# Kernel optimization log

Measured on AMD Instinct MI355X. Metric: run time of the kernel, lower is better.

## Reference

```python
import jax, jax.numpy as jnp
import numpy as np

EPS = 1e-5
SIGMA = 1.0

def _conv(x, w, stride):
    return jax.lax.conv_general_dilated(
        x, w, window_strides=(stride, stride),
        padding=[(w.shape[2] // 2, w.shape[2] // 2), (w.shape[3] // 2, w.shape[3] // 2)],
        dimension_numbers=('NCHW', 'OIHW', 'NCHW'))

def _bn(x, gamma, beta, mean, var):
    # inference-mode batchnorm over channel dim (NCHW)
    inv = gamma / jnp.sqrt(var + EPS)
    return x * inv[None, :, None, None] + (beta - mean * inv)[None, :, None, None]

def setup_inputs() -> dict:
    key = jax.random.key(0)
    ks = jax.random.split(key, 8)
    B, M, H, W, K = 8, 128, 64, 64, 6
    x = jax.random.normal(ks[0], (B, M, H, W), jnp.float32)
    cf = jax.random.normal(ks[1], (B, M, H, W), jnp.float32)
    w1 = jax.random.normal(ks[2], (M // 2, M, 3, 3), jnp.float32) * 0.05
    w2 = jax.random.normal(ks[3], (M // 4, M // 2, 3, 3), jnp.float32) * 0.05
    w3 = jax.random.normal(ks[4], (K, M // 4, 1, 1), jnp.float32) * 0.05
    def bn_params(k, c):
        k1, k2 = jax.random.split(k)
        return (jnp.ones((c,), jnp.float32),
                jnp.zeros((c,), jnp.float32),
                jax.random.normal(k1, (c,), jnp.float32) * 0.1,
                jnp.abs(jax.random.normal(k2, (c,), jnp.float32)) * 0.1 + 1.0)
    g1, b1, m1, v1 = bn_params(ks[5], M // 2)
    g2, b2, m2, v2 = bn_params(ks[6], M // 4)
    g3, b3, m3, v3 = bn_params(ks[7], K)
    return dict(x=x, center_features=cf, w1=w1, g1=g1, b1=b1, m1=m1, v1=v1,
                w2=w2, g2=g2, b2=b2, m2=m2, v2=v2,
                w3=w3, g3=g3, b3=b3, m3=m3, v3=v3)

def reference(x, center_features, w1, g1, b1, m1, v1, w2, g2, b2, m2, v2, w3, g3, b3, m3, v3):
    # center branch: conv-bn-relu x2 (stride 2) + 1x1 conv-bn, then spatial mean
    c = jax.nn.relu(_bn(_conv(center_features, w1, 2), g1, b1, m1, v1))
    c = jax.nn.relu(_bn(_conv(c, w2, 2), g2, b2, m2, v2))
    c = _bn(_conv(c, w3, 1), g3, b3, m3, v3)
    centers = c.reshape(c.shape[0], c.shape[1], -1).mean(axis=2)  # [B, K]

    B, C, H, W = x.shape
    K = centers.shape[-1]
    xf = x.reshape(B, C, H * W, 1)                      # [B,C,HW,1]
    cb = centers[:, None, None, :]                      # [B,1,1,K]
    dist = (xf - cb) ** 2                               # [B,C,HW,K]
    phi_soft = jax.nn.softmax(-SIGMA * dist, axis=-1)
    qsoft = jnp.sum(phi_soft * cb, axis=-1).reshape(B, C, H, W)
    symbols = jnp.argmin(dist, axis=-1)                 # [B,C,HW] (== argmax of hard softmax)
    qhard = centers[jnp.arange(B)[:, None, None], symbols].reshape(B, C, H, W)
    qbar = qsoft + jax.lax.stop_gradient(qhard - qsoft)
    return qbar, qsoft, qhard, symbols.reshape(B, C, H, W), centers
```

## Files before the change

### kernel.cpp

```cpp
#include <hip/hip_runtime.h>
#include <math.h>

#define BN_EPS 1e-5
#define SIGMA 1.0f

typedef double f64x4 __attribute__((ext_vector_type(4)));

__global__ __launch_bounds__(256, 4) void conv1_mfma_kernel(
    const float* __restrict__ in, const float* __restrict__ w1,
    float* __restrict__ part)
{
    __shared__ float swt[9216];

    int bid = blockIdx.x;
    int mt  = bid & 15;
    int b   = (bid >> 4) & 7;
    int ksp = bid >> 7;

    int tid = threadIdx.x;
    int l   = tid & 63;
    int wv  = tid >> 6;
    int wm  = wv >> 1;
    int wn  = wv & 1;
    int lc  = l & 15;
    int lg  = l >> 4;

    double ap = (double)lc;
    double bp = (l == 0) ? 1.0 : 0.0;
    f64x4 dp = {0., 0., 0., 0.};
    dp = __builtin_amdgcn_mfma_f64_16x16x4f64(ap, bp, dp, 0, 0, 0);
    int row0[4];
    #pragma unroll
    for (int r = 0; r < 4; ++r)
        row0[r] = ((int)__shfl(dp[r], (l & 0x30), 64)) & 15;

    for (int i = tid; i < 9216; i += 256) {
        int g   = i & 3;
        int n   = (i >> 2) & 63;
        int kic = i >> 8;
        int khw = kic >> 2;
        int icb = kic & 3;
        swt[i] = w1[(n * 128 + ksp * 16 + icb * 4 + g) * 9 + khw];
    }
    __syncthreads();

    f64x4 d00 = {0., 0., 0., 0.}, d01 = {0., 0., 0., 0.};
    f64x4 d10 = {0., 0., 0., 0.}, d11 = {0., 0., 0., 0.};

    const float* cb = in + (size_t)(b * 128 + ksp * 16 + lg) * 4096;
    int r0 = 4 * mt + 2 * wm - 1;
    const float* pbase = cb + (ptrdiff_t)(r0 * 64 + 2 * lc - 1);
    bool c0ok = (lc != 0);

    const float* pB = swt + (wn * 32 + lc) * 4 + lg;

    #pragma unroll
    for (int khw = 0; khw < 9; ++khw) {
        const int kh = khw / 3;
        const int kw = khw - 3 * kh;
        bool rowok = (kh > 0) || (r0 >= 0);
        #pragma unroll
        for (int icb = 0; icb < 4; ++icb) {
            const int offA = icb * 16384 + kh * 64 + kw;
            bool ok0 = rowok && ((kw > 0) || c0ok);
            const float* q0 = ok0 ? (pbase + offA) : cb;
            float f0 = *q0;
            double a0 = ok0 ? (double)f0 : 0.0;
            const float* q1 = rowok ? (pbase + offA + 32) : cb;
            float f1 = *q1;
            double a1 = rowok ? (double)f1 : 0.0;

            const int offB = (khw * 4 + icb) * 256;
            double b0 = (double)pB[offB];
            double b1 = (double)pB[offB + 64];

            d00 = __builtin_amdgcn_mfma_f64_16x16x4f64(a0, b0, d00, 0, 0, 0);
            d01 = __builtin_amdgcn_mfma_f64_16x16x4f64(a0, b1, d01, 0, 0, 0);
            d10 = __builtin_amdgcn_mfma_f64_16x16x4f64(a1, b0, d10, 0, 0, 0);
            d11 = __builtin_amdgcn_mfma_f64_16x16x4f64(a1, b1, d11, 0, 0, 0);
        }
    }

    __syncthreads();
    float* so = swt;
    #pragma unroll
    for (int mi = 0; mi < 2; ++mi) {
        f64x4 v0 = mi ? d10 : d00;
        f64x4 v1 = mi ? d11 : d01;
        #pragma unroll
        for (int r = 0; r < 4; ++r) {
            int m   = wm * 32 + mi * 16 + row0[r];
            int oc0 = wn * 32 + lc;
            so[oc0 * 65 + m]        = (float)v0[r];
            so[(oc0 + 16) * 65 + m] = (float)v1[r];
        }
    }
    __syncthreads();
    int oh0 = 2 * mt;
    for (int i = tid; i < 4096; i += 256) {
        int oc = i >> 6;
        int m  = i & 63;
        part[(size_t)ksp * 524288 +
             ((b * 64 + oc) * 32 + oh0 + (m >> 5)) * 32 + (m & 31)] = so[oc * 65 + m];
    }
}

__global__ __launch_bounds__(256) void conv2_partial_kernel(
    const float* __restrict__ part1,
    const float* __restrict__ g1, const float* __restrict__ be1,
    const float* __restrict__ mn1, const float* __restrict__ vr1,
    const float* __restrict__ w,
    float* __restrict__ part)
{
    __shared__ float tin[4][33][36];
    __shared__ float twt[4][9][8];
    __shared__ double sinv[4], ssh[4];

    int bid = blockIdx.x;
    int ocg = bid & 3;
    int b   = (bid >> 2) & 7;
    int isp = bid >> 5;

    int tid = threadIdx.x;
    int ow  = tid & 15;
    int oh  = tid >> 4;

    if (tid < 4) {
        int ch = isp * 4 + tid;
        double inv = (double)g1[ch] / sqrt((double)vr1[ch] + BN_EPS);
        sinv[tid] = inv;
        ssh[tid]  = (double)be1[ch] - (double)mn1[ch] * inv;
    }
    __syncthreads();

    for (int lin = tid; lin < 4 * 33 * 34; lin += 256) {
        int c   = lin % 34;
        int t2  = lin / 34;
        int rr  = t2 % 33;
        int icc = t2 / 33;
        int ih  = rr - 1;
        int iw  = c - 1;
        float v = 0.f;
        if ((unsigned)ih < 32u && (unsigned)iw < 32u) {
            int ch  = isp * 4 + icc;
            int idx = ((b * 64 + ch) * 32 + ih) * 32 + iw;
            double s = 0.0;
            #pragma unroll
            for (int p = 0; p < 8; ++p) s += (double)part1[idx + p * 524288];
            double o = s * sinv[icc] + ssh[icc];
            v = fmaxf((float)o, 0.f);
        }
        tin[icc][rr][c] = v;
    }
    for (int i = tid; i < 288; i += 256) {
        int j   = i & 7;
        int k   = (i >> 3) % 9;
        int icc = i / 72;
        twt[icc][k][j] = w[(ocg * 8 + j) * 576 + (isp * 4 + icc) * 9 + k];
    }
    __syncthreads();

    double acc[8];
    #pragma unroll
    for (int j = 0; j < 8; ++j) acc[j] = 0.0;

    for (int icc = 0; icc < 4; ++icc) {
        double xv[9];
        #pragma unroll
        for (int kh = 0; kh < 3; ++kh)
            #pragma unroll
            for (int kw = 0; kw < 3; ++kw)
                xv[kh * 3 + kw] = (double)tin[icc][2 * oh + kh][2 * ow + kw];
        #pragma unroll
        for (int k = 0; k < 9; ++k) {
            float4 wa = *(const float4*)&twt[icc][k][0];
            float4 wb = *(const float4*)&twt[icc][k][4];
            acc[0] = fma(xv[k], (double)wa.x, acc[0]);
            acc[1] = fma(xv[k], (double)wa.y, acc[1]);
            acc[2] = fma(xv[k], (double)wa.z, acc[2]);
            acc[3] = fma(xv[k], (double)wa.w, acc[3]);
            acc[4] = fma(xv[k], (double)wb.x, acc[4]);
            acc[5] = fma(xv[k], (double)wb.y, acc[5]);
            acc[6] = fma(xv[k], (double)wb.z, acc[6]);
            acc[7] = fma(xv[k], (double)wb.w, acc[7]);
        }
    }
    int obase = ((b * 32 + ocg * 8) * 16 + oh) * 16 + ow;
    #pragma unroll
    for (int j = 0; j < 8; ++j)
        part[isp * 65536 + obase + j * 256] = (float)acc[j];
}

__global__ __launch_bounds__(256) void conv2_combine_ybar_kernel(
    const float* __restrict__ part,
    const float* __restrict__ g, const float* __restrict__ be,
    const float* __restrict__ mn, const float* __restrict__ vr,
    double* __restrict__ ybar)
{
    __shared__ double sm[4];
    int j  = blockIdx.x;
    int oc = j & 31;
    int t  = threadIdx.x;
    int idx = j * 256 + t;
    double s = 0.0;
    #pragma unroll
    for (int p = 0; p < 16; ++p) s += (double)part[idx + p * 65536];
    double inv = (double)g[oc] / sqrt((double)vr[oc] + BN_EPS);
    double o = s * inv + ((double)be[oc] - (double)mn[oc] * inv);
    double v = fmax(o, 0.0);
    #pragma unroll
    for (int off = 32; off > 0; off >>= 1) v += __shfl_down(v, off, 64);
    if ((t & 63) == 0) sm[t >> 6] = v;
    __syncthreads();
    if (t == 0) ybar[j] = (sm[0] + sm[1] + sm[2] + sm[3]) * (1.0 / 256.0);
}

__global__ __launch_bounds__(64) void centers_kernel(
    const double* __restrict__ ybar, const float* __restrict__ w3,
    const float* __restrict__ g, const float* __restrict__ be,
    const float* __restrict__ mn, const float* __restrict__ vr,
    double* __restrict__ cen_ws, float* __restrict__ cen_out)
{
    int t = threadIdx.x;
    if (t < 48) {
        int b = t / 6;
        int k = t % 6;
        double acc = 0.0;
        for (int ic = 0; ic < 32; ++ic) acc = fma((double)w3[k * 32 + ic], ybar[b * 32 + ic], acc);
        double inv = (double)g[k] / sqrt((double)vr[k] + BN_EPS);
        double c = acc * inv + ((double)be[k] - (double)mn[k] * inv);
        cen_ws[t]  = c;
        cen_out[t] = (float)c;
    }
}

__global__ __launch_bounds__(256) void quant_kernel(
    const float* __restrict__ x, const double* __restrict__ centers,
    float* __restrict__ qbar, float* __restrict__ qsoft,
    float* __restrict__ qhard, float* __restrict__ sym)
{
    int vid = blockIdx.x * 256 + threadIdx.x;
    int b = vid >> 17;

    double c[6];
    float cf[6];
    #pragma unroll
    for (int k = 0; k < 6; ++k) { c[k] = centers[b * 6 + k]; cf[k] = (float)c[k]; }

    float4 xv = ((const float4*)x)[vid];
    float xs[4] = {xv.x, xv.y, xv.z, xv.w};
    float r_bar[4], r_soft[4], r_hard[4], r_sym[4];

    #pragma unroll
    for (int i = 0; i < 4; ++i) {
        double xx = (double)xs[i];
        double d[6];
        double dmin = 1e300;
        int amin = 0;
        #pragma unroll
        for (int k = 0; k < 6; ++k) {
            double t = xx - c[k];
            d[k] = t * t;
            if (d[k] < dmin) { dmin = d[k]; amin = k; }
        }
        float se = 0.f, sw = 0.f;
        #pragma unroll
        for (int k = 0; k < 6; ++k) {
            float e = __expf(SIGMA * (float)(dmin - d[k]));
            se += e;
            sw += e * cf[k];
        }
        float qs = sw / se;
        float qh = cf[amin];
        r_soft[i] = qs;
        r_hard[i] = qh;
        r_bar[i]  = qh;
        r_sym[i]  = (float)amin;
    }

    ((float4*)qbar)[vid]  = make_float4(r_bar[0],  r_bar[1],  r_bar[2],  r_bar[3]);
    ((float4*)qsoft)[vid] = make_float4(r_soft[0], r_soft[1], r_soft[2], r_soft[3]);
    ((float4*)qhard)[vid] = make_float4(r_hard[0], r_hard[1], r_hard[2], r_hard[3]);
    ((float4*)sym)[vid]   = make_float4(r_sym[0],  r_sym[1],  r_sym[2],  r_sym[3]);
}

extern "C" void kernel_launch(void* const* d_in, const int* in_sizes, int n_in,
                              void* d_out, int out_size, void* d_ws, size_t ws_size,
                              hipStream_t stream) {
    const float* x  = (const float*)d_in[0];
    const float* cf = (const float*)d_in[1];
    const float* w1 = (const float*)d_in[2];
    const float* g1 = (const float*)d_in[3];
    const float* b1 = (const float*)d_in[4];
    const float* m1 = (const float*)d_in[5];
    const float* v1 = (const float*)d_in[6];
    const float* w2 = (const float*)d_in[7];
    const float* g2 = (const float*)d_in[8];
    const float* b2 = (const float*)d_in[9];
    const float* m2 = (const float*)d_in[10];
    const float* v2 = (const float*)d_in[11];
    const float* w3 = (const float*)d_in[12];
    const float* g3 = (const float*)d_in[13];
    const float* b3 = (const float*)d_in[14];
    const float* m3 = (const float*)d_in[15];
    const float* v3 = (const float*)d_in[16];

    const int NELEM = 8 * 128 * 64 * 64;
    float* out   = (float*)d_out;
    float* qbar  = out;
    float* qsoft = out + (size_t)NELEM;
    float* qhard = out + (size_t)2 * NELEM;
    float* sym   = out + (size_t)3 * NELEM;
    float* cen_o = out + (size_t)4 * NELEM;

    char* ws = (char*)d_ws;
    float*  part1 = (float*)(ws);
    float*  part2 = (float*)(ws + 16777216);
    double* yb    = (double*)(ws + 20971520);
    double* cen   = (double*)(ws + 20973568);

    conv1_mfma_kernel<<<1024, 256, 0, stream>>>(cf, w1, part1);
    conv2_partial_kernel<<<512, 256, 0, stream>>>(part1, g1, b1, m1, v1, w2, part2);
    conv2_combine_ybar_kernel<<<256, 256, 0, stream>>>(part2, g2, b2, m2, v2, yb);
    centers_kernel<<<1, 64, 0, stream>>>(yb, w3, g3, b3, m3, v3, cen, cen_o);
    quant_kernel<<<NELEM / 4 / 256, 256, 0, stream>>>(x, cen, qbar, qsoft, qhard, sym);
}
```

Before: 187.9 us.

## Split conv1 work between FP64 MFMA blocks and scalar FP64 FMA blocks

Conv1 now launches a hybrid grid. Half the blocks keep the FP64 MFMA path for input-channel splits 4-7. The other half compute splits 0-3 with scalar double FMAs: weights are staged in LDS as doubles and input rows are register-prefetched. The aim is to use both the MFMA units and the vector ALUs at once, since the FP64 matrix path alone caps throughput. The cost is a scalar path with heavy register use and uneven per-block work, which could unbalance the blocks or lower occupancy.

```diff
diff --git a/kernel.cpp b/kernel.cpp
--- a/kernel.cpp
+++ b/kernel.cpp
@@ -6,102 +6,191 @@
 
 typedef double f64x4 __attribute__((ext_vector_type(4)));
 
-__global__ __launch_bounds__(256, 4) void conv1_mfma_kernel(
+__global__ __launch_bounds__(256, 4) void conv1_hybrid_kernel(
     const float* __restrict__ in, const float* __restrict__ w1,
     float* __restrict__ part)
 {
-    __shared__ float swt[9216];
-
-    int bid = blockIdx.x;
-    int mt  = bid & 15;
-    int b   = (bid >> 4) & 7;
-    int ksp = bid >> 7;
-
-    int tid = threadIdx.x;
-    int l   = tid & 63;
-    int wv  = tid >> 6;
-    int wm  = wv >> 1;
-    int wn  = wv & 1;
-    int lc  = l & 15;
-    int lg  = l >> 4;
-
-    double ap = (double)lc;
-    double bp = (l == 0) ? 1.0 : 0.0;
-    f64x4 dp = {0., 0., 0., 0.};
-    dp = __builtin_amdgcn_mfma_f64_16x16x4f64(ap, bp, dp, 0, 0, 0);
-    int row0[4];
-    #pragma unroll
-    for (int r = 0; r < 4; ++r)
-        row0[r] = ((int)__shfl(dp[r], (l & 0x30), 64)) & 15;
-
-    for (int i = tid; i < 9216; i += 256) {
-        int g   = i & 3;
-        int n   = (i >> 2) & 63;
-        int kic = i >> 8;
-        int khw = kic >> 2;
-        int icb = kic & 3;
-        swt[i] = w1[(n * 128 + ksp * 16 + icb * 4 + g) * 9 + khw];
-    }
-    __syncthreads();
-
-    f64x4 d00 = {0., 0., 0., 0.}, d01 = {0., 0., 0., 0.};
-    f64x4 d10 = {0., 0., 0., 0.}, d11 = {0., 0., 0., 0.};
-
-    const float* cb = in + (size_t)(b * 128 + ksp * 16 + lg) * 4096;
-    int r0 = 4 * mt + 2 * wm - 1;
-    const float* pbase = cb + (ptrdiff_t)(r0 * 64 + 2 * lc - 1);
-    bool c0ok = (lc != 0);
-
-    const float* pB = swt + (wn * 32 + lc) * 4 + lg;
-
-    #pragma unroll
-    for (int khw = 0; khw < 9; ++khw) {
-        const int kh = khw / 3;
-        const int kw = khw - 3 * kh;
-        bool rowok = (kh > 0) || (r0 >= 0);
-        #pragma unroll
-        for (int icb = 0; icb < 4; ++icb) {
-            const int offA = icb * 16384 + kh * 64 + kw;
-            bool ok0 = rowok && ((kw > 0) || c0ok);
-            const float* q0 = ok0 ? (pbase + offA) : cb;
-            float f0 = *q0;
-            double a0 = ok0 ? (double)f0 : 0.0;
-            const float* q1 = rowok ? (pbase + offA + 32) : cb;
-            float f1 = *q1;
-            double a1 = rowok ? (double)f1 : 0.0;
-
-            const int offB = (khw * 4 + icb) * 256;
-            double b0 = (double)pB[offB];
-            double b1 = (double)pB[offB + 64];
-
-            d00 = __builtin_amdgcn_mfma_f64_16x16x4f64(a0, b0, d00, 0, 0, 0);
-            d01 = __builtin_amdgcn_mfma_f64_16x16x4f64(a0, b1, d01, 0, 0, 0);
-            d10 = __builtin_amdgcn_mfma_f64_16x16x4f64(a1, b0, d10, 0, 0, 0);
-            d11 = __builtin_amdgcn_mfma_f64_16x16x4f64(a1, b1, d11, 0, 0, 0);
-        }
-    }
-
-    __syncthreads();
-    float* so = swt;
-    #pragma unroll
-    for (int mi = 0; mi < 2; ++mi) {
-        f64x4 v0 = mi ? d10 : d00;
-        f64x4 v1 = mi ? d11 : d01;
-        #pragma unroll
-        for (int r = 0; r < 4; ++r) {
-            int m   = wm * 32 + mi * 16 + row0[r];
-            int oc0 = wn * 32 + lc;
-            so[oc0 * 65 + m]        = (float)v0[r];
-            so[(oc0 + 16) * 65 + m] = (float)v1[r];
-        }
-    }
-    __syncthreads();
-    int oh0 = 2 * mt;
-    for (int i = tid; i < 4096; i += 256) {
-        int oc = i >> 6;
-        int m  = i & 63;
-        part[(size_t)ksp * 524288 +
-             ((b * 64 + oc) * 32 + oh0 + (m >> 5)) * 32 + (m & 31)] = so[oc * 65 + m];
+    __shared__ double smem_d[4608];
+
+    int bid  = blockIdx.x;
+    int typ  = (bid >> 3) & 1;
+    int bid2 = ((bid >> 4) << 3) | (bid & 7);
+    int tid  = threadIdx.x;
+
+    if (typ == 0) {
+        double* wlds = smem_d;
+        int oht = bid2 & 1;
+        int b   = (bid2 >> 1) & 7;
+        int isp = (bid2 >> 4) & 3;
+        int ocg = bid2 >> 6;
+
+        int ow  = tid & 31;
+        int ohp = tid >> 5;
+        int oh0 = oht * 16 + ohp * 2;
+        int ih0 = 2 * oh0 - 1;
+        int iw0 = 2 * ow - 1;
+
+        for (int i = tid; i < 1152; i += 256) {
+            int j  = i & 7;
+            int t  = i >> 3;
+            int k  = t % 9;
+            int ic = t / 9;
+            wlds[i] = (double)w1[((ocg * 8 + j) * 128 + isp * 16 + ic) * 9 + k];
+        }
+        __syncthreads();
+
+        double acc0[8], acc1[8];
+        #pragma unroll
+        for (int j = 0; j < 8; ++j) { acc0[j] = 0.0; acc1[j] = 0.0; }
+
+        bool rowok[5], colok[3];
+        #pragma unroll
+        for (int t = 0; t < 5; ++t) rowok[t] = (ih0 + t) >= 0;
+        #pragma unroll
+        for (int t = 0; t < 3; ++t) colok[t] = (iw0 + t) >= 0;
+
+        const float* base0 = in + ((size_t)(b * 128 + isp * 16) * 64 + ih0) * 64 + iw0;
+
+        float cur[15];
+        #pragma unroll
+        for (int t = 0; t < 5; ++t)
+            #pragma unroll
+            for (int kw = 0; kw < 3; ++kw)
+                cur[t * 3 + kw] = (rowok[t] && colok[kw]) ? base0[t * 64 + kw] : 0.f;
+
+        for (int ic = 0; ic < 16; ++ic) {
+            float nxt[15];
+            if (ic + 1 < 16) {
+                const float* basen = base0 + (size_t)(ic + 1) * 4096;
+                #pragma unroll
+                for (int t = 0; t < 5; ++t)
+                    #pragma unroll
+                    for (int kw = 0; kw < 3; ++kw)
+                        nxt[t * 3 + kw] = (rowok[t] && colok[kw]) ? basen[t * 64 + kw] : 0.f;
+            }
+            double xv[15];
+            #pragma unroll
+            for (int i = 0; i < 15; ++i) xv[i] = (double)cur[i];
+
+            const double* wk = &wlds[ic * 72];
+            #pragma unroll
+            for (int k = 0; k < 9; ++k) {
+                int kh = k / 3, kw = k % 3;
+                double2 wa = *(const double2*)&wk[k * 8 + 0];
+                double2 wb2 = *(const double2*)&wk[k * 8 + 2];
+                double2 wc = *(const double2*)&wk[k * 8 + 4];
+                double2 wd = *(const double2*)&wk[k * 8 + 6];
+                double x0 = xv[kh * 3 + kw];
+                double x1 = xv[(kh + 2) * 3 + kw];
+                acc0[0] = fma(x0, wa.x, acc0[0]);   acc1[0] = fma(x1, wa.x, acc1[0]);
+                acc0[1] = fma(x0, wa.y, acc0[1]);   acc1[1] = fma(x1, wa.y, acc1[1]);
+                acc0[2] = fma(x0, wb2.x, acc0[2]);  acc1[2] = fma(x1, wb2.x, acc1[2]);
+                acc0[3] = fma(x0, wb2.y, acc0[3]);  acc1[3] = fma(x1, wb2.y, acc1[3]);
+                acc0[4] = fma(x0, wc.x, acc0[4]);   acc1[4] = fma(x1, wc.x, acc1[4]);
+                acc0[5] = fma(x0, wc.y, acc0[5]);   acc1[5] = fma(x1, wc.y, acc1[5]);
+                acc0[6] = fma(x0, wd.x, acc0[6]);   acc1[6] = fma(x1, wd.x, acc1[6]);
+                acc0[7] = fma(x0, wd.y, acc0[7]);   acc1[7] = fma(x1, wd.y, acc1[7]);
+            }
+            #pragma unroll
+            for (int i = 0; i < 15; ++i) cur[i] = nxt[i];
+        }
+
+        #pragma unroll
+        for (int j = 0; j < 8; ++j) {
+            int idx0 = ((b * 64 + ocg * 8 + j) * 32 + oh0) * 32 + ow;
+            part[(size_t)isp * 524288 + idx0]      = (float)acc0[j];
+            part[(size_t)isp * 524288 + idx0 + 32] = (float)acc1[j];
+        }
+    } else {
+        float* swt = (float*)smem_d;
+        int mt  = bid2 & 15;
+        int b   = (bid2 >> 4) & 7;
+        int ksp = 4 + (bid2 >> 7);
+
+        int l   = tid & 63;
+        int wv  = tid >> 6;
+        int wm  = wv >> 1;
+        int wn  = wv & 1;
+        int lc  = l & 15;
+        int lg  = l >> 4;
+
+        double ap = (double)lc;
+        double bp = (l == 0) ? 1.0 : 0.0;
+        f64x4 dpr = {0., 0., 0., 0.};
+        dpr = __builtin_amdgcn_mfma_f64_16x16x4f64(ap, bp, dpr, 0, 0, 0);
+        int row0[4];
+        #pragma unroll
+        for (int r = 0; r < 4; ++r)
+            row0[r] = ((int)__shfl(dpr[r], (l & 0x30), 64)) & 15;
+
+        for (int i = tid; i < 9216; i += 256) {
+            int g   = i & 3;
+            int n   = (i >> 2) & 63;
+            int kic = i >> 8;
+            int khw = kic >> 2;
+            int icb = kic & 3;
+            swt[i] = w1[(n * 128 + ksp * 16 + icb * 4 + g) * 9 + khw];
+        }
+        __syncthreads();
+
+        f64x4 d00 = {0., 0., 0., 0.}, d01 = {0., 0., 0., 0.};
+        f64x4 d10 = {0., 0., 0., 0.}, d11 = {0., 0., 0., 0.};
+
+        const float* cb = in + (size_t)(b * 128 + ksp * 16 + lg) * 4096;
+        int r0 = 4 * mt + 2 * wm - 1;
+        const float* pbase = cb + (ptrdiff_t)(r0 * 64 + 2 * lc - 1);
+        bool c0ok = (lc != 0);
+        const float* pB = swt + (wn * 32 + lc) * 4 + lg;
+
+        #pragma unroll
+        for (int khw = 0; khw < 9; ++khw) {
+            const int kh = khw / 3;
+            const int kw = khw - 3 * kh;
+            bool rowok = (kh > 0) || (r0 >= 0);
+            #pragma unroll
+            for (int icb = 0; icb < 4; ++icb) {
+                const int offA = icb * 16384 + kh * 64 + kw;
+                bool ok0 = rowok && ((kw > 0) || c0ok);
+                const float* q0 = ok0 ? (pbase + offA) : cb;
+                float f0 = *q0;
+                double a0 = ok0 ? (double)f0 : 0.0;
+                const float* q1 = rowok ? (pbase + offA + 32) : cb;
+                float f1 = *q1;
+                double a1 = rowok ? (double)f1 : 0.0;
+
+                const int offB = (khw * 4 + icb) * 256;
+                double b0 = (double)pB[offB];
+                double b1 = (double)pB[offB + 64];
+
+                d00 = __builtin_amdgcn_mfma_f64_16x16x4f64(a0, b0, d00, 0, 0, 0);
+                d01 = __builtin_amdgcn_mfma_f64_16x16x4f64(a0, b1, d01, 0, 0, 0);
+                d10 = __builtin_amdgcn_mfma_f64_16x16x4f64(a1, b0, d10, 0, 0, 0);
+                d11 = __builtin_amdgcn_mfma_f64_16x16x4f64(a1, b1, d11, 0, 0, 0);
+            }
+        }
+
+        __syncthreads();
+        float* so = (float*)smem_d;
+        #pragma unroll
+        for (int mi = 0; mi < 2; ++mi) {
+            f64x4 v0 = mi ? d10 : d00;
+            f64x4 v1 = mi ? d11 : d01;
+            #pragma unroll
+            for (int r = 0; r < 4; ++r) {
+                int m   = wm * 32 + mi * 16 + row0[r];
+                int oc0 = wn * 32 + lc;
+                so[oc0 * 66 + m]        = (float)v0[r];
+                so[(oc0 + 16) * 66 + m] = (float)v1[r];
+            }
+        }
+        __syncthreads();
+        int oh0 = 2 * mt;
+        for (int i = tid; i < 4096; i += 256) {
+            int oc = i >> 6;
+            int m  = i & 63;
+            part[(size_t)ksp * 524288 +
+                 ((b * 64 + oc) * 32 + oh0 + (m >> 5)) * 32 + (m & 31)] = so[oc * 66 + m];
+        }
     }
 }
 
@@ -319,7 +408,7 @@
     double* yb    = (double*)(ws + 20971520);
     double* cen   = (double*)(ws + 20973568);
 
-    conv1_mfma_kernel<<<1024, 256, 0, stream>>>(cf, w1, part1);
+    conv1_hybrid_kernel<<<1024, 256, 0, stream>>>(cf, w1, part1);
     conv2_partial_kernel<<<512, 256, 0, stream>>>(part1, g1, b1, m1, v1, w2, part2);
     conv2_combine_ybar_kernel<<<256, 256, 0, stream>>>(part2, g2, b2, m2, v2, yb);
     centers_kernel<<<1, 64, 0, stream>>>(yb, w3, g3, b3, m3, v3, cen, cen_o);
```

After: 188.0 us. No clear change (+0.0%).
